# Performance work log

Measured on AMD Instinct MI355X. Metric: run time of the kernel, lower is better.

Reference implementation:

```python
import jax, jax.numpy as jnp
import numpy as np


def setup_inputs() -> dict:
    key = jax.random.key(0)
    ks = jax.random.split(key, 8)
    B, C, H, W = 8, 64, 64, 64
    C2 = C // 2
    return {
        "x": jax.random.normal(ks[0], (B, C, H, W), dtype=jnp.float32),
        "Wq": jax.random.normal(ks[1], (C2, C), dtype=jnp.float32) * 0.1,
        "bq": jax.random.normal(ks[2], (C2,), dtype=jnp.float32) * 0.01,
        "Wk": jax.random.normal(ks[3], (C2, C), dtype=jnp.float32) * 0.1,
        "bk": jax.random.normal(ks[4], (C2,), dtype=jnp.float32) * 0.01,
        "Wv": jax.random.normal(ks[5], (C, C), dtype=jnp.float32) * 0.1,
        "bv": jax.random.normal(ks[6], (C,), dtype=jnp.float32) * 0.01,
        "sigma": jnp.float32(1.0),
    }


def reference(x, Wq, bq, Wk, bk, Wv, bv, sigma):
    B, C, H, W = x.shape
    N = H * W
    xf = x.reshape(B, C, N)  # flatten spatial
    # 1x1 convs == per-pixel linear projections over channels
    q = jnp.einsum("oc,bcn->bon", Wq, xf) + bq[None, :, None]  # [B, C/2, N]
    k = jnp.einsum("oc,bcn->bon", Wk, xf) + bk[None, :, None]  # [B, C/2, N]
    v = jnp.einsum("oc,bcn->bon", Wv, xf) + bv[None, :, None]  # [B, C,   N]
    # pairwise squared L2 distance via expansion: |q|^2 + |k|^2 - 2 q.k
    q_sq = jnp.sum(q * q, axis=1)  # [B, N]
    k_sq = jnp.sum(k * k, axis=1)  # [B, N]
    qk = jnp.einsum("bcn,bcm->bnm", q, k)  # [B, N, N]
    dist_sq = q_sq[:, :, None] + k_sq[:, None, :] - 2.0 * qk
    similarity = jnp.exp(-dist_sq / (2.0 * sigma * sigma))  # RBF kernel
    attention = jax.nn.softmax(similarity, axis=-1)  # [B, N, N]
    # attn @ v^T -> [B, N, C]
    attention_out = jnp.einsum("bnm,bcm->bnc", attention, v)
    # faithful to torch .view(B, C, H, W) on a [B, N, C] tensor (raw reshape)
    attention_out = attention_out.reshape(B, C, H, W)
    return x + attention_out
```

## Files before the change

kernel.cpp:

```cpp
#include <hip/hip_runtime.h>
#include <hip/hip_bf16.h>

typedef __attribute__((ext_vector_type(2))) _Float16 f16x2;
typedef __attribute__((ext_vector_type(4))) _Float16 f16x4;
typedef __attribute__((ext_vector_type(8))) _Float16 f16x8;
typedef __attribute__((ext_vector_type(4))) float f32x4;

#define B_ 8
#define N_ 4096
#define C_ 64
#define CQ_ 32
#define SPLIT 4
#define KEYS (N_ / SPLIT)
#define NT (KEYS / 64)
#define QB 128

#define L2E_ 1.4426950408889634f
#define LOG2L_ 0.5287663729448977f

#define P0_ 0.9992f
#define P1_ 0.70591f
#define P2_ 0.20093f
#define P3_ 0.094395f

__device__ __forceinline__ void async16(void* lds, const void* gsrc) {
    __builtin_amdgcn_global_load_lds(
        (const __attribute__((address_space(1))) unsigned int*)gsrc,
        (__attribute__((address_space(3))) unsigned int*)lds, 16, 0, 0);
}

__device__ __forceinline__ f16x2 wpoly(float z0, float z1) {
    f16x2 h = __builtin_bit_cast(f16x2, __builtin_amdgcn_cvt_pkrtz(z0, z1));
    const _Float16 c3 = (_Float16)P3_, c2 = (_Float16)P2_;
    const _Float16 c1 = (_Float16)P1_, c0 = (_Float16)P0_;
    return ((h * c3 + c2) * h + c1) * h + c0;
}

__global__ __launch_bounds__(256) void proj_kernel(
    const float* __restrict__ x,
    const float* __restrict__ Wq, const float* __restrict__ bq,
    const float* __restrict__ Wk, const float* __restrict__ bk,
    const float* __restrict__ Wv, const float* __restrict__ bv,
    const float* __restrict__ sigp,
    _Float16* __restrict__ qh, _Float16* __restrict__ khf,
    _Float16* __restrict__ vhf,
    float* __restrict__ nqs, float* __restrict__ nkf)
{
    __shared__ __align__(16) _Float16 xs16[64][72];
    __shared__ __align__(16) _Float16 vtmp[64][76];

    const int t = threadIdx.x;
    const int wid = __builtin_amdgcn_readfirstlane(t >> 6);
    const int l = t & 63;
    const int lg = l >> 4;
    const int lm = l & 15;
    const int b = blockIdx.x >> 6;
    const int tile = blockIdx.x & 63;
    const int n0 = tile * 64;
    const size_t bN = (size_t)b * N_;

    {
        const int c = t >> 2, pq = t & 3;
        const float* xp = x + (bN * C_ / N_ * 0 + ((size_t)b * C_ + c) * N_) + n0 + pq * 16;
        f32x4 a0 = *(const f32x4*)(xp);
        f32x4 a1 = *(const f32x4*)(xp + 4);
        f32x4 a2 = *(const f32x4*)(xp + 8);
        f32x4 a3 = *(const f32x4*)(xp + 12);
        #pragma unroll
        for (int i = 0; i < 4; ++i) {
            xs16[pq * 16 + i][c]      = (_Float16)a0[i];
            xs16[pq * 16 + 4 + i][c]  = (_Float16)a1[i];
            xs16[pq * 16 + 8 + i][c]  = (_Float16)a2[i];
            xs16[pq * 16 + 12 + i][c] = (_Float16)a3[i];
        }
    }
    __syncthreads();

    const float* Wr;
    const float* br;
    if (wid == 0)      { Wr = Wq;            br = bq; }
    else if (wid == 1) { Wr = Wk;            br = bk; }
    else if (wid == 2) { Wr = Wv;            br = bv; }
    else               { Wr = Wv + 32 * 64;  br = bv + 32; }

    f16x8 af[2][2];
    #pragma unroll
    for (int og = 0; og < 2; ++og) {
        #pragma unroll
        for (int ks = 0; ks < 2; ++ks) {
            const float* wp = Wr + (og * 16 + lm) * 64 + ks * 32 + lg * 8;
            const f32x4 w0 = *(const f32x4*)(wp);
            const f32x4 w1 = *(const f32x4*)(wp + 4);
            f16x8 h;
            #pragma unroll
            for (int e = 0; e < 4; ++e) { h[e] = (_Float16)w0[e]; h[4 + e] = (_Float16)w1[e]; }
            af[og][ks] = h;
        }
    }
    f32x4 bias[2];
    #pragma unroll
    for (int og = 0; og < 2; ++og)
        bias[og] = *(const f32x4*)(br + og * 16 + lg * 4);

    f32x4 d[2][4];
    #pragma unroll
    for (int pg = 0; pg < 4; ++pg) {
        const f16x8 bf0 = *(const f16x8*)(&xs16[pg * 16 + lm][lg * 8]);
        const f16x8 bf1 = *(const f16x8*)(&xs16[pg * 16 + lm][32 + lg * 8]);
        #pragma unroll
        for (int og = 0; og < 2; ++og) {
            f32x4 acc = __builtin_amdgcn_mfma_f32_16x16x32_f16(af[og][0], bf0, bias[og], 0, 0, 0);
            d[og][pg] = __builtin_amdgcn_mfma_f32_16x16x32_f16(af[og][1], bf1, acc, 0, 0, 0);
        }
    }

    const float sv = sigp[0];
    const float cdL = 0.7213475204444817f / (sv * sv);
    const float c1 = 2.0f * cdL;

    if (wid < 2) {
        float s[4];
        #pragma unroll
        for (int pg = 0; pg < 4; ++pg) {
            float acc = 0.f;
            #pragma unroll
            for (int og = 0; og < 2; ++og)
                #pragma unroll
                for (int r = 0; r < 4; ++r)
                    acc = fmaf(d[og][pg][r], d[og][pg][r], acc);
            acc += __shfl_xor(acc, 16);
            acc += __shfl_xor(acc, 32);
            s[pg] = acc;
        }
        if (wid == 0) {
            #pragma unroll
            for (int og = 0; og < 2; ++og) {
                #pragma unroll
                for (int pg = 0; pg < 4; ++pg) {
                    f16x4 h;
                    #pragma unroll
                    for (int r = 0; r < 4; ++r) h[r] = (_Float16)(d[og][pg][r] * c1);
                    *(f16x4*)(qh + (bN + n0 + pg * 16 + lm) * CQ_ + og * 16 + lg * 4) = h;
                }
            }
            if (l < 16) {
                #pragma unroll
                for (int pg = 0; pg < 4; ++pg)
                    nqs[bN + n0 + pg * 16 + l] = LOG2L_ - s[pg] * cdL;
            }
        } else {
            const size_t tbase = ((size_t)b * (N_ / 64) + tile) * 4;
            #pragma unroll
            for (int og = 0; og < 2; ++og) {
                const int g = og * 2 + (lg >> 1);
                const int e0 = (lg & 1) * 4;
                #pragma unroll
                for (int pg = 0; pg < 4; ++pg) {
                    f16x4 h;
                    #pragma unroll
                    for (int r = 0; r < 4; ++r) h[r] = (_Float16)d[og][pg][r];
                    *(f16x4*)(khf + (tbase + g) * 512 + (pg * 16 + lm) * 8 + e0) = h;
                }
            }
            if (l < 16) {
                #pragma unroll
                for (int pg = 0; pg < 4; ++pg) {
                    const int kkg = n0 + pg * 16 + l;
                    const int kk = kkg & 31;
                    const int kap = (((kk & 15) >> 2) << 3) + (kk & 3) + (((kk >> 4) & 1) << 2);
                    nkf[((size_t)b * (N_ / 32) + (kkg >> 5)) * 32 + kap] = -s[pg] * cdL;
                }
            }
        }
    } else {
        const int co = (wid - 2) * 32;
        #pragma unroll
        for (int og = 0; og < 2; ++og)
            #pragma unroll
            for (int pg = 0; pg < 4; ++pg)
                #pragma unroll
                for (int r = 0; r < 4; ++r)
                    vtmp[co + og * 16 + lg * 4 + r][pg * 16 + lm] = (_Float16)d[og][pg][r];
    }
    __syncthreads();

    #pragma unroll
    for (int p = 0; p < 2; ++p) {
        const int jg = (t >> 6) + p * 4;
        const int ch = t & 63;
        const int p0 = (jg >> 2) * 32 + (jg & 3) * 4;
        const f16x4 a0 = *(const f16x4*)(&vtmp[ch][p0]);
        const f16x4 a1 = *(const f16x4*)(&vtmp[ch][p0 + 16]);
        f16x8 hv;
        #pragma unroll
        for (int e = 0; e < 4; ++e) { hv[e] = a0[e]; hv[4 + e] = a1[e]; }
        *(f16x8*)(vhf + ((size_t)b * (N_ / 64) + tile) * 4096 + (size_t)(jg * 64 + ch) * 8) = hv;
    }
}

__global__ __launch_bounds__(256, 4) void attn_kernel(
    const _Float16* __restrict__ qh,
    const _Float16* __restrict__ khf,
    const _Float16* __restrict__ vhf,
    const float* __restrict__ nqs,
    const float* __restrict__ nkf,
    _Float16* __restrict__ opart,
    float* __restrict__ dpart)
{
    __shared__ __align__(16) _Float16 Kb[3][2048];
    __shared__ __align__(16) _Float16 Vb[3][4096];
    __shared__ __align__(16) float sNkAll[1024];

    const int t = threadIdx.x;
    const int wid = t >> 6;
    const int l = t & 63;
    const int lg = l >> 4;
    const int lm = l & 15;

    const int orig = blockIdx.x;
    const int wgid = (orig & 7) * 128 + (orig >> 3);
    const int qblk = wgid & 31;
    const int fam = wgid >> 5;
    const int split = fam & (SPLIT - 1);
    const int b = fam >> 2;
    const int qbase = qblk * QB + wid * 32;
    const int k0 = split * KEYS;
    const size_t bN = (size_t)b * N_;

    const f16x8 qfA = *(const f16x8*)(qh + (bN + qbase + lm) * CQ_ + 8 * lg);
    const f16x8 qfB = *(const f16x8*)(qh + (bN + qbase + 16 + lm) * CQ_ + 8 * lg);
    const float nqA = nqs[bN + qbase + lm];
    const float nqB = nqs[bN + qbase + 16 + lm];

    const _Float16* kg = khf + ((size_t)b * (N_ / 64) + (k0 >> 6)) * 2048 + wid * 512 + l * 8;
    const _Float16* vg = vhf + ((size_t)b * (N_ / 64) + (k0 >> 6)) * 4096 + wid * 1024 + l * 8;
    const float* nkp = nkf + bN + k0 + wid * 256 + l * 4;

    f32x4 accA[4], accB[4], accdA, accdB;
    #pragma unroll
    for (int i = 0; i < 4; ++i) {
        accA[i] = (f32x4){0.f, 0.f, 0.f, 0.f};
        accB[i] = (f32x4){0.f, 0.f, 0.f, 0.f};
    }
    accdA = (f32x4){0.f, 0.f, 0.f, 0.f};
    accdB = (f32x4){0.f, 0.f, 0.f, 0.f};
    f16x8 ones;
    #pragma unroll
    for (int e = 0; e < 8; ++e) ones[e] = (_Float16)1.0f;

    f16x8 paJ0A, paJ0B, paJ1A, paJ1B;

    auto ISSUE = [&](int tile, int bf) {
        async16(&Kb[bf][wid * 512],        kg + (size_t)tile * 2048);
        async16(&Vb[bf][wid * 1024],       vg + (size_t)tile * 4096);
        async16(&Vb[bf][wid * 1024 + 512], vg + (size_t)tile * 4096 + 512);
    };

    auto HALF = [&](int J, int tt, int ck, int cv, bool doPV, f16x8& pA, f16x8& pB) {
        const f16x8 kf0 = *(const f16x8*)(&Kb[ck][(lg * 64 + J * 32 + lm) * 8]);
        const f16x8 kf1 = *(const f16x8*)(&Kb[ck][(lg * 64 + J * 32 + 16 + lm) * 8]);
        const f32x4 NK0 = *(const f32x4*)(&sNkAll[tt * 64 + J * 32 + lg * 8]);
        const f32x4 NK1 = *(const f32x4*)(&sNkAll[tt * 64 + J * 32 + lg * 8 + 4]);
        f32x4 CA0, CA1, CB0, CB1;
        #pragma unroll
        for (int r = 0; r < 4; ++r) {
            CA0[r] = NK0[r] + nqA; CA1[r] = NK1[r] + nqA;
            CB0[r] = NK0[r] + nqB; CB1[r] = NK1[r] + nqB;
        }
        __builtin_amdgcn_s_setprio(1);
        const f32x4 SA0 = __builtin_amdgcn_mfma_f32_16x16x32_f16(kf0, qfA, CA0, 0, 0, 0);
        const f32x4 SA1 = __builtin_amdgcn_mfma_f32_16x16x32_f16(kf1, qfA, CA1, 0, 0, 0);
        const f32x4 SB0 = __builtin_amdgcn_mfma_f32_16x16x32_f16(kf0, qfB, CB0, 0, 0, 0);
        const f32x4 SB1 = __builtin_amdgcn_mfma_f32_16x16x32_f16(kf1, qfB, CB1, 0, 0, 0);
        __builtin_amdgcn_s_setprio(0);
        if (doPV) {
            __builtin_amdgcn_s_setprio(1);
            #pragma unroll
            for (int tc = 0; tc < 4; ++tc) {
                const f16x8 vf = *(const f16x8*)(&Vb[cv][((J * 4 + lg) * 64 + tc * 16 + lm) * 8]);
                accA[tc] = __builtin_amdgcn_mfma_f32_16x16x32_f16(pA, vf, accA[tc], 0, 0, 0);
                accB[tc] = __builtin_amdgcn_mfma_f32_16x16x32_f16(pB, vf, accB[tc], 0, 0, 0);
            }
            accdA = __builtin_amdgcn_mfma_f32_16x16x32_f16(pA, ones, accdA, 0, 0, 0);
            accdB = __builtin_amdgcn_mfma_f32_16x16x32_f16(pB, ones, accdB, 0, 0, 0);
            __builtin_amdgcn_s_setprio(0);
        }
        f16x2 w;
        w = wpoly(__builtin_amdgcn_exp2f(SA0[0]), __builtin_amdgcn_exp2f(SA0[1])); pA[0] = w[0]; pA[1] = w[1];
        w = wpoly(__builtin_amdgcn_exp2f(SA0[2]), __builtin_amdgcn_exp2f(SA0[3])); pA[2] = w[0]; pA[3] = w[1];
        w = wpoly(__builtin_amdgcn_exp2f(SA1[0]), __builtin_amdgcn_exp2f(SA1[1])); pA[4] = w[0]; pA[5] = w[1];
        w = wpoly(__builtin_amdgcn_exp2f(SA1[2]), __builtin_amdgcn_exp2f(SA1[3])); pA[6] = w[0]; pA[7] = w[1];
        w = wpoly(__builtin_amdgcn_exp2f(SB0[0]), __builtin_amdgcn_exp2f(SB0[1])); pB[0] = w[0]; pB[1] = w[1];
        w = wpoly(__builtin_amdgcn_exp2f(SB0[2]), __builtin_amdgcn_exp2f(SB0[3])); pB[2] = w[0]; pB[3] = w[1];
        w = wpoly(__builtin_amdgcn_exp2f(SB1[0]), __builtin_amdgcn_exp2f(SB1[1])); pB[4] = w[0]; pB[5] = w[1];
        w = wpoly(__builtin_amdgcn_exp2f(SB1[2]), __builtin_amdgcn_exp2f(SB1[3])); pB[6] = w[0]; pB[7] = w[1];
    };

    async16(&sNkAll[wid * 256], nkp);
    ISSUE(0, 0);
    asm volatile("s_waitcnt vmcnt(0)" ::: "memory");
    asm volatile("s_barrier" ::: "memory");
    ISSUE(1, 1);
    HALF(0, 0, 0, 0, false, paJ0A, paJ0B);
    HALF(1, 0, 0, 0, false, paJ1A, paJ1B);

    int cv = 0, ck = 1, ib = 2;
    #pragma unroll 1
    for (int tt = 1; tt < NT; ++tt) {
        asm volatile("s_waitcnt vmcnt(0)" ::: "memory");
        asm volatile("s_barrier" ::: "memory");
        if (tt + 1 < NT) ISSUE(tt + 1, ib);
        HALF(0, tt, ck, cv, true, paJ0A, paJ0B);
        HALF(1, tt, ck, cv, true, paJ1A, paJ1B);
        const int tmp = cv; cv = ck; ck = ib; ib = tmp;
    }

    __builtin_amdgcn_s_setprio(1);
    #pragma unroll
    for (int J = 0; J < 2; ++J) {
        const f16x8& pA = J ? paJ1A : paJ0A;
        const f16x8& pB = J ? paJ1B : paJ0B;
        #pragma unroll
        for (int tc = 0; tc < 4; ++tc) {
            const f16x8 vf = *(const f16x8*)(&Vb[cv][((J * 4 + lg) * 64 + tc * 16 + lm) * 8]);
            accA[tc] = __builtin_amdgcn_mfma_f32_16x16x32_f16(pA, vf, accA[tc], 0, 0, 0);
            accB[tc] = __builtin_amdgcn_mfma_f32_16x16x32_f16(pB, vf, accB[tc], 0, 0, 0);
        }
        accdA = __builtin_amdgcn_mfma_f32_16x16x32_f16(pA, ones, accdA, 0, 0, 0);
        accdB = __builtin_amdgcn_mfma_f32_16x16x32_f16(pB, ones, accdB, 0, 0, 0);
    }
    __builtin_amdgcn_s_setprio(0);

    const size_t obA = ((size_t)split * B_ + b) * N_ + qbase;
    if (lm == 0) {
        #pragma unroll
        for (int r = 0; r < 4; ++r) {
            dpart[obA + lg * 4 + r] = accdA[r];
            dpart[obA + 16 + lg * 4 + r] = accdB[r];
        }
    }
    #pragma unroll
    for (int tc = 0; tc < 4; ++tc) {
        #pragma unroll
        for (int r = 0; r < 4; ++r) {
            opart[(obA + lg * 4 + r) * C_ + tc * 16 + lm] = (_Float16)accA[tc][r];
            opart[(obA + 16 + lg * 4 + r) * C_ + tc * 16 + lm] = (_Float16)accB[tc][r];
        }
    }
}

__global__ __launch_bounds__(256) void combine_kernel(
    const float* __restrict__ x,
    const _Float16* __restrict__ opart,
    const float* __restrict__ dpart,
    float* __restrict__ out)
{
    const int gid = blockIdx.x * 256 + threadIdx.x;
    const int c0 = (gid & 7) * 8;
    const int bn = gid >> 3;

    float den = 0.f;
    #pragma unroll
    for (int s = 0; s < SPLIT; ++s) den += dpart[(size_t)s * B_ * N_ + bn];
    const float rden = 1.0f / den;

    float o[8] = {0.f, 0.f, 0.f, 0.f, 0.f, 0.f, 0.f, 0.f};
    #pragma unroll
    for (int s = 0; s < SPLIT; ++s) {
        const f16x8 h = *(const f16x8*)(opart + (((size_t)s * B_ * N_ + bn) * C_ + c0));
        #pragma unroll
        for (int e = 0; e < 8; ++e) o[e] += (float)h[e];
    }

    const size_t base = (size_t)bn * C_ + c0;
    const f32x4 x0 = *(const f32x4*)(x + base);
    const f32x4 x1 = *(const f32x4*)(x + base + 4);
    f32x4 r0, r1;
    #pragma unroll
    for (int e = 0; e < 4; ++e) {
        r0[e] = x0[e] + o[e] * rden;
        r1[e] = x1[e] + o[e + 4] * rden;
    }
    *(f32x4*)(out + base) = r0;
    *(f32x4*)(out + base + 4) = r1;
}

extern "C" void kernel_launch(void* const* d_in, const int* in_sizes, int n_in,
                              void* d_out, int out_size, void* d_ws, size_t ws_size,
                              hipStream_t stream) {
    const float* x   = (const float*)d_in[0];
    const float* Wq  = (const float*)d_in[1];
    const float* bq  = (const float*)d_in[2];
    const float* Wk  = (const float*)d_in[3];
    const float* bk  = (const float*)d_in[4];
    const float* Wv  = (const float*)d_in[5];
    const float* bv  = (const float*)d_in[6];
    const float* sig = (const float*)d_in[7];
    float* out = (float*)d_out;

    char* ws = (char*)d_ws;
    _Float16* qh   = (_Float16*)(ws);
    _Float16* khf  = (_Float16*)(ws + (2u << 20));
    _Float16* vhf  = (_Float16*)(ws + (4u << 20));
    float*   nqs   = (float*)(ws + (8u << 20));
    float*   nkf   = (float*)(ws + (8u << 20) + (128u << 10));
    _Float16* opart = (_Float16*)(ws + (8u << 20) + (256u << 10));
    float*   dpart = (float*)(ws + (24u << 20) + (256u << 10));

    proj_kernel<<<512, 256, 0, stream>>>(x, Wq, bq, Wk, bk, Wv, bv, sig,
                                         qh, khf, vhf, nqs, nkf);
    attn_kernel<<<1024, 256, 0, stream>>>(qh, khf, vhf, nqs, nkf, opart, dpart);
    combine_kernel<<<(B_ * N_ * 8) / 256, 256, 0, stream>>>(x, opart, dpart, out);
}
```

Baseline: 55.95 us.

## Fuse split-K combine into attention kernel via last-arriving-block atomic counter

Removes the separate combine kernel launch. Each attention workgroup atomically increments a per-(batch, query-block) counter after writing its partial outputs. The last of the SPLIT workgroups then reduces the partial numerators and denominators and writes the residual output. The counters are zeroed by the projection kernel. This saves a kernel launch and its tail, and lets the combine overlap with other attention blocks, at the cost of extra fences and atomics in every block.

```diff
diff --git a/kernel.cpp b/kernel.cpp
--- a/kernel.cpp
+++ b/kernel.cpp
@@ -44,7 +44,8 @@
     const float* __restrict__ sigp,
     _Float16* __restrict__ qh, _Float16* __restrict__ khf,
     _Float16* __restrict__ vhf,
-    float* __restrict__ nqs, float* __restrict__ nkf)
+    float* __restrict__ nqs, float* __restrict__ nkf,
+    int* __restrict__ cnt)
 {
     __shared__ __align__(16) _Float16 xs16[64][72];
     __shared__ __align__(16) _Float16 vtmp[64][76];
@@ -59,9 +60,11 @@
     const int n0 = tile * 64;
     const size_t bN = (size_t)b * N_;
 
+    if (blockIdx.x == 0) cnt[t] = 0;
+
     {
         const int c = t >> 2, pq = t & 3;
-        const float* xp = x + (bN * C_ / N_ * 0 + ((size_t)b * C_ + c) * N_) + n0 + pq * 16;
+        const float* xp = x + ((size_t)b * C_ + c) * N_ + n0 + pq * 16;
         f32x4 a0 = *(const f32x4*)(xp);
         f32x4 a1 = *(const f32x4*)(xp + 4);
         f32x4 a2 = *(const f32x4*)(xp + 8);
@@ -199,17 +202,21 @@
 }
 
 __global__ __launch_bounds__(256, 4) void attn_kernel(
+    const float* __restrict__ x,
     const _Float16* __restrict__ qh,
     const _Float16* __restrict__ khf,
     const _Float16* __restrict__ vhf,
     const float* __restrict__ nqs,
     const float* __restrict__ nkf,
     _Float16* __restrict__ opart,
-    float* __restrict__ dpart)
+    float* __restrict__ dpart,
+    int* __restrict__ cnt,
+    float* __restrict__ out)
 {
     __shared__ __align__(16) _Float16 Kb[3][2048];
     __shared__ __align__(16) _Float16 Vb[3][4096];
     __shared__ __align__(16) float sNkAll[1024];
+    __shared__ int sdone;
 
     const int t = threadIdx.x;
     const int wid = t >> 6;
@@ -347,42 +354,48 @@
             opart[(obA + 16 + lg * 4 + r) * C_ + tc * 16 + lm] = (_Float16)accB[tc][r];
         }
     }
-}
-
-__global__ __launch_bounds__(256) void combine_kernel(
-    const float* __restrict__ x,
-    const _Float16* __restrict__ opart,
-    const float* __restrict__ dpart,
-    float* __restrict__ out)
-{
-    const int gid = blockIdx.x * 256 + threadIdx.x;
-    const int c0 = (gid & 7) * 8;
-    const int bn = gid >> 3;
-
-    float den = 0.f;
-    #pragma unroll
-    for (int s = 0; s < SPLIT; ++s) den += dpart[(size_t)s * B_ * N_ + bn];
-    const float rden = 1.0f / den;
-
-    float o[8] = {0.f, 0.f, 0.f, 0.f, 0.f, 0.f, 0.f, 0.f};
-    #pragma unroll
-    for (int s = 0; s < SPLIT; ++s) {
-        const f16x8 h = *(const f16x8*)(opart + (((size_t)s * B_ * N_ + bn) * C_ + c0));
-        #pragma unroll
-        for (int e = 0; e < 8; ++e) o[e] += (float)h[e];
-    }
-
-    const size_t base = (size_t)bn * C_ + c0;
-    const f32x4 x0 = *(const f32x4*)(x + base);
-    const f32x4 x1 = *(const f32x4*)(x + base + 4);
-    f32x4 r0, r1;
-    #pragma unroll
-    for (int e = 0; e < 4; ++e) {
-        r0[e] = x0[e] + o[e] * rden;
-        r1[e] = x1[e] + o[e + 4] * rden;
-    }
-    *(f32x4*)(out + base) = r0;
-    *(f32x4*)(out + base + 4) = r1;
+
+    __syncthreads();
+    __threadfence();
+    __syncthreads();
+    if (t == 0) {
+        const int old = atomicAdd(&cnt[b * 32 + qblk], 1);
+        sdone = (old == SPLIT - 1) ? 1 : 0;
+    }
+    __syncthreads();
+    if (sdone) {
+        __threadfence();
+        const int nb0 = qblk * QB;
+        #pragma unroll
+        for (int u = 0; u < 4; ++u) {
+            const int unit = u * 256 + t;
+            const int row = unit >> 3;
+            const int c0 = (unit & 7) * 8;
+            const size_t bn = bN + nb0 + row;
+            float den = 0.f;
+            #pragma unroll
+            for (int s = 0; s < SPLIT; ++s) den += dpart[(size_t)s * B_ * N_ + bn];
+            const float rden = 1.0f / den;
+            float o[8] = {0.f, 0.f, 0.f, 0.f, 0.f, 0.f, 0.f, 0.f};
+            #pragma unroll
+            for (int s = 0; s < SPLIT; ++s) {
+                const f16x8 h = *(const f16x8*)(opart + (((size_t)s * B_ * N_ + bn) * C_ + c0));
+                #pragma unroll
+                for (int e = 0; e < 8; ++e) o[e] += (float)h[e];
+            }
+            const size_t base = bn * C_ + c0;
+            const f32x4 x0 = *(const f32x4*)(x + base);
+            const f32x4 x1 = *(const f32x4*)(x + base + 4);
+            f32x4 r0, r1;
+            #pragma unroll
+            for (int e = 0; e < 4; ++e) {
+                r0[e] = x0[e] + o[e] * rden;
+                r1[e] = x1[e] + o[e + 4] * rden;
+            }
+            *(f32x4*)(out + base) = r0;
+            *(f32x4*)(out + base + 4) = r1;
+        }
+    }
 }
 
 extern "C" void kernel_launch(void* const* d_in, const int* in_sizes, int n_in,
@@ -406,9 +419,10 @@
     float*   nkf   = (float*)(ws + (8u << 20) + (128u << 10));
     _Float16* opart = (_Float16*)(ws + (8u << 20) + (256u << 10));
     float*   dpart = (float*)(ws + (24u << 20) + (256u << 10));
+    int*     cnt   = (int*)(ws + (24u << 20) + (768u << 10));
 
     proj_kernel<<<512, 256, 0, stream>>>(x, Wq, bq, Wk, bk, Wv, bv, sig,
-                                         qh, khf, vhf, nqs, nkf);
-    attn_kernel<<<1024, 256, 0, stream>>>(qh, khf, vhf, nqs, nkf, opart, dpart);
-    combine_kernel<<<(B_ * N_ * 8) / 256, 256, 0, stream>>>(x, opart, dpart, out);
+                                         qh, khf, vhf, nqs, nkf, cnt);
+    attn_kernel<<<1024, 256, 0, stream>>>(x, qh, khf, vhf, nqs, nkf,
+                                          opart, dpart, cnt, out);
 }
```

Result: slower. 191.7 us (+242.7%).
